# Kernel optimization log

Hardware: AMD Instinct MI355X
Metric: run time of the kernel (lower is better)

## Reference

```python
import jax, jax.numpy as jnp
import numpy as np
from jax import lax

IN_CH, HID, OUT_CH, N_MID, BATCH = 16, 8, 4, 60, 4194304


def setup_inputs() -> dict:
    key = jax.random.key(0)
    ks = jax.random.split(key, 7)
    scale = 1.0 / jnp.sqrt(jnp.float32(HID))  # keep 62-layer linear chain numerically stable
    x = jax.random.normal(ks[0], (BATCH, IN_CH), dtype=jnp.float32)
    W1 = jax.random.normal(ks[1], (HID, IN_CH), dtype=jnp.float32) * scale
    b1 = jax.random.normal(ks[2], (HID,), dtype=jnp.float32) * 0.01
    Ws = jax.random.normal(ks[3], (N_MID, HID, HID), dtype=jnp.float32) * scale
    bs = jax.random.normal(ks[4], (N_MID, HID), dtype=jnp.float32) * 0.01
    W2 = jax.random.normal(ks[5], (OUT_CH, HID), dtype=jnp.float32) * scale
    b2 = jax.random.normal(ks[6], (OUT_CH,), dtype=jnp.float32) * 0.01
    return {"x": x, "W1": W1, "b1": b1, "Ws": Ws, "bs": bs, "W2": W2, "b2": b2}


def reference(x, W1, b1, Ws, bs, W2, b2):
    # fc1: [B,16] -> [B,8]  (torch Linear: x @ W.T + b)
    h = x @ W1.T + b1

    # 60 sequential 8x8 Linear layers, no activation; scan over layer axis
    def step(h, wb):
        w, b = wb
        return h @ w.T + b, None

    h, _ = lax.scan(step, h, (Ws, bs))

    # fc2: [B,8] -> [B,4]
    return h @ W2.T + b2
```

## Files before the change

### kernel.cpp

```cpp
#include <hip/hip_runtime.h>

#define IN_CH  16
#define HID    8
#define OUT_CH 4
#define N_MID  60
#define BATCH  4194304

__global__ __launch_bounds__(128) void fold_kernel(
    const float* __restrict__ W1, const float* __restrict__ b1,
    const float* __restrict__ Ws, const float* __restrict__ bs,
    const float* __restrict__ W2, const float* __restrict__ b2,
    float* __restrict__ Mc ) {

    __shared__ float A[2][HID][IN_CH];
    __shared__ float d[2][HID];

    const int t   = threadIdx.x;
    const int r   = t >> 4;
    const int col = t & 15;

    A[0][r][col] = W1[r * IN_CH + col];
    if (t < HID) d[0][t] = b1[t];
    __syncthreads();

    int cur = 0;
    for (int l = 0; l < N_MID; ++l) {
        const float* W = Ws + l * HID * HID;
        float acc = 0.f;
        #pragma unroll
        for (int k = 0; k < HID; ++k)
            acc += W[r * HID + k] * A[cur][k][col];
        A[1 - cur][r][col] = acc;
        if (t < HID) {
            float bc = bs[l * HID + t];
            #pragma unroll
            for (int k = 0; k < HID; ++k)
                bc += W[t * HID + k] * d[cur][k];
            d[1 - cur][t] = bc;
        }
        cur = 1 - cur;
        __syncthreads();
    }

    if (t < OUT_CH * IN_CH) {
        const int rr = t >> 4, cc = t & 15;
        float acc = 0.f;
        #pragma unroll
        for (int k = 0; k < HID; ++k)
            acc += W2[rr * HID + k] * A[cur][k][cc];
        Mc[rr * IN_CH + cc] = acc;
    }
    if (t < OUT_CH) {
        float acc = b2[t];
        #pragma unroll
        for (int k = 0; k < HID; ++k)
            acc += W2[t * HID + k] * d[cur][k];
        Mc[OUT_CH * IN_CH + t] = acc;
    }
}

__global__ __launch_bounds__(256) void apply_kernel(
    const float* __restrict__ x,
    const float* __restrict__ Mc,
    float* __restrict__ out) {

    __shared__ float sM[OUT_CH * IN_CH + OUT_CH];
    if (threadIdx.x < OUT_CH * IN_CH + OUT_CH) sM[threadIdx.x] = Mc[threadIdx.x];
    __syncthreads();

    const size_t i = (size_t)blockIdx.x * blockDim.x + threadIdx.x;
    if (i >= (size_t)BATCH) return;

    const float4* xp = (const float4*)(x + i * IN_CH);
    float4 v0 = xp[0], v1 = xp[1], v2 = xp[2], v3 = xp[3];
    float xv[IN_CH] = { v0.x, v0.y, v0.z, v0.w,
                        v1.x, v1.y, v1.z, v1.w,
                        v2.x, v2.y, v2.z, v2.w,
                        v3.x, v3.y, v3.z, v3.w };

    float o[OUT_CH];
    #pragma unroll
    for (int rr = 0; rr < OUT_CH; ++rr) {
        float acc = sM[OUT_CH * IN_CH + rr];
        #pragma unroll
        for (int k = 0; k < IN_CH; ++k)
            acc += sM[rr * IN_CH + k] * xv[k];
        o[rr] = acc;
    }
    ((float4*)out)[i] = make_float4(o[0], o[1], o[2], o[3]);
}

extern "C" void kernel_launch(void* const* d_in, const int* in_sizes, int n_in,
                              void* d_out, int out_size, void* d_ws, size_t ws_size,
                              hipStream_t stream) {
    const float* x  = (const float*)d_in[0];
    const float* W1 = (const float*)d_in[1];
    const float* b1 = (const float*)d_in[2];
    const float* Ws = (const float*)d_in[3];
    const float* bs = (const float*)d_in[4];
    const float* W2 = (const float*)d_in[5];
    const float* b2 = (const float*)d_in[6];
    float* out = (float*)d_out;
    float* Mc  = (float*)d_ws;

    fold_kernel<<<1, 128, 0, stream>>>(W1, b1, Ws, bs, W2, b2, Mc);

    const int threads = 256;
    const int blocks  = BATCH / threads;
    apply_kernel<<<blocks, threads, 0, stream>>>(x, Mc, out);
}
```

Baseline: 420.5 us.

## Split each row across four lanes with shuffle reduction; stage weights in LDS

The apply kernel now gives each batch row to four consecutive threads. Each thread loads one float4 of x, which makes the loads fully coalesced and contiguous. The thread computes partial dot products for all four outputs, reduces them with xor shuffles, and writes the one output matching its lane. Weights are read from global memory into registers, which removes the LDS staging and the block barrier. The fold kernel also preloads all 60 layer weights and biases into shared memory to cut global-load latency in its serial chain. The cost is four times as many threads plus the extra shuffle work.

```diff
diff --git a/kernel.cpp b/kernel.cpp
--- a/kernel.cpp
+++ b/kernel.cpp
@@ -12,6 +12,8 @@
     const float* __restrict__ W2, const float* __restrict__ b2,
     float* __restrict__ Mc ) {
 
+    __shared__ float sWs[N_MID * HID * HID];
+    __shared__ float sbs[N_MID * HID];
     __shared__ float A[2][HID][IN_CH];
     __shared__ float d[2][HID];
 
@@ -19,20 +21,23 @@
     const int r   = t >> 4;
     const int col = t & 15;
 
+    for (int i = t; i < N_MID * HID * HID; i += 128) sWs[i] = Ws[i];
+    for (int i = t; i < N_MID * HID;       i += 128) sbs[i] = bs[i];
+
     A[0][r][col] = W1[r * IN_CH + col];
     if (t < HID) d[0][t] = b1[t];
     __syncthreads();
 
     int cur = 0;
     for (int l = 0; l < N_MID; ++l) {
-        const float* W = Ws + l * HID * HID;
+        const float* W = sWs + l * HID * HID;
         float acc = 0.f;
         #pragma unroll
         for (int k = 0; k < HID; ++k)
             acc += W[r * HID + k] * A[cur][k][col];
         A[1 - cur][r][col] = acc;
         if (t < HID) {
-            float bc = bs[l * HID + t];
+            float bc = sbs[l * HID + t];
             #pragma unroll
             for (int k = 0; k < HID; ++k)
                 bc += W[t * HID + k] * d[cur][k];
@@ -64,30 +69,31 @@
     const float* __restrict__ Mc,
     float* __restrict__ out) {
 
-    __shared__ float sM[OUT_CH * IN_CH + OUT_CH];
-    if (threadIdx.x < OUT_CH * IN_CH + OUT_CH) sM[threadIdx.x] = Mc[threadIdx.x];
-    __syncthreads();
+    const int tid = threadIdx.x;
+    const size_t g = (size_t)blockIdx.x * 256 + tid;
+    const int q = tid & 3;
 
-    const size_t i = (size_t)blockIdx.x * blockDim.x + threadIdx.x;
-    if (i >= (size_t)BATCH) return;
+    const float4* M4 = (const float4*)Mc;
+    const float4 m0 = M4[0 * 4 + q];
+    const float4 m1 = M4[1 * 4 + q];
+    const float4 m2 = M4[2 * 4 + q];
+    const float4 m3 = M4[3 * 4 + q];
+    const float  cb = Mc[OUT_CH * IN_CH + q];
 
-    const float4* xp = (const float4*)(x + i * IN_CH);
-    float4 v0 = xp[0], v1 = xp[1], v2 = xp[2], v3 = xp[3];
-    float xv[IN_CH] = { v0.x, v0.y, v0.z, v0.w,
-                        v1.x, v1.y, v1.z, v1.w,
-                        v2.x, v2.y, v2.z, v2.w,
-                        v3.x, v3.y, v3.z, v3.w };
+    const float4 xv = ((const float4*)x)[g];
 
-    float o[OUT_CH];
-    #pragma unroll
-    for (int rr = 0; rr < OUT_CH; ++rr) {
-        float acc = sM[OUT_CH * IN_CH + rr];
-        #pragma unroll
-        for (int k = 0; k < IN_CH; ++k)
-            acc += sM[rr * IN_CH + k] * xv[k];
-        o[rr] = acc;
-    }
-    ((float4*)out)[i] = make_float4(o[0], o[1], o[2], o[3]);
+    float p0 = m0.x * xv.x + m0.y * xv.y + m0.z * xv.z + m0.w * xv.w;
+    float p1 = m1.x * xv.x + m1.y * xv.y + m1.z * xv.z + m1.w * xv.w;
+    float p2 = m2.x * xv.x + m2.y * xv.y + m2.z * xv.z + m2.w * xv.w;
+    float p3 = m3.x * xv.x + m3.y * xv.y + m3.z * xv.z + m3.w * xv.w;
+
+    p0 += __shfl_xor(p0, 1); p1 += __shfl_xor(p1, 1);
+    p2 += __shfl_xor(p2, 1); p3 += __shfl_xor(p3, 1);
+    p0 += __shfl_xor(p0, 2); p1 += __shfl_xor(p1, 2);
+    p2 += __shfl_xor(p2, 2); p3 += __shfl_xor(p3, 2);
+
+    const float val = (q == 0 ? p0 : q == 1 ? p1 : q == 2 ? p2 : p3) + cb;
+    out[g] = val;
 }
 
 extern "C" void kernel_launch(void* const* d_in, const int* in_sizes, int n_in,
@@ -105,7 +111,6 @@
 
     fold_kernel<<<1, 128, 0, stream>>>(W1, b1, Ws, bs, W2, b2, Mc);
 
-    const int threads = 256;
-    const int blocks  = BATCH / threads;
-    apply_kernel<<<blocks, threads, 0, stream>>>(x, Mc, out);
+    const int blocks = (BATCH * (IN_CH / 4)) / 256;
+    apply_kernel<<<blocks, 256, 0, stream>>>(x, Mc, out);
 }
```

After: 396.0 us. 1.06x faster.
